# Optimization experiments

Measured on AMD Instinct MI355X. Metric: run time of the kernel, lower is better.

The kernel has to match this reference:

```python
import jax, jax.numpy as jnp
import numpy as np

N_NODES = 50000
N_EDGES = 800000
IN_DIM, HID_DIM, OUT_DIM = 512, 64, 40


def setup_inputs() -> dict:
    key = jax.random.key(0)
    k1, k2, k3, k4, k5 = jax.random.split(key, 5)
    x = jax.random.normal(k1, (N_NODES, IN_DIM), dtype=jnp.float32)
    src = jax.random.randint(k2, (N_EDGES,), 0, N_NODES, dtype=jnp.int64)
    dst = jax.random.randint(k3, (N_EDGES,), 0, N_NODES, dtype=jnp.int64)
    # Linear weights stored as [in, out] (equivalent to torch W.T), no bias.
    W1 = jax.random.normal(k4, (IN_DIM, HID_DIM), dtype=jnp.float32) * (1.0 / np.sqrt(IN_DIM))
    W2 = jax.random.normal(k5, (HID_DIM, OUT_DIM), dtype=jnp.float32) * (1.0 / np.sqrt(HID_DIM))
    return {"x": x, "src": src, "dst": dst, "W1": W1, "W2": W2}


def _gnn_layer(x, src, dst, W, n_nodes):
    # linear projection then sparse-adjacency aggregation:
    # out[i] = sum_{(j->i) in E} (x @ W)[j]
    h = x @ W                                   # [N, out_dim]
    return jax.ops.segment_sum(h[src], dst, num_segments=n_nodes)


def reference(x, src, dst, W1, W2):
    n = x.shape[0]
    h = _gnn_layer(x, src, dst, W1, n)          # [N, HID]
    h = jax.nn.relu(h)
    h = _gnn_layer(h, src, dst, W2, n)          # [N, OUT]
    return jax.nn.log_softmax(h, axis=1)
```

## Files before the change

kernel.cpp:

```cpp
#include <hip/hip_runtime.h>
#include <hip/hip_bf16.h>
#include <math.h>

constexpr int IN_DIM = 512;
constexpr int HID = 64;
constexpr int OUTD = 40;
constexpr int CAP = 64;

typedef __attribute__((ext_vector_type(8))) short bf16x8;
typedef __attribute__((ext_vector_type(4))) float floatx4;
typedef unsigned short ushort_t;

__device__ __forceinline__ unsigned short f2bf(float f) {
    unsigned u = __float_as_uint(f);
    u += 0x7fff + ((u >> 16) & 1);
    return (unsigned short)(u >> 16);
}

__device__ __forceinline__ unsigned pk2(float x, float y) {
    __hip_bfloat162 h = __float22bfloat162_rn(make_float2(x, y));
    return *reinterpret_cast<unsigned*>(&h);
}

#define GW4 asm volatile("s_waitcnt vmcnt(4)" ::: "memory")
#define GW0 asm volatile("s_waitcnt vmcnt(0)" ::: "memory")

__global__ __launch_bounds__(256) void w1t_fill_kernel(const float* __restrict__ W1,
                                                       const float* __restrict__ W2,
                                                       ushort_t* __restrict__ Wt,
                                                       ushort_t* __restrict__ W2tb,
                                                       const int* __restrict__ src,
                                                       const int* __restrict__ dst,
                                                       int* __restrict__ deg,
                                                       int* __restrict__ srcs, int E, int N) {
    int bid = blockIdx.x;
    if (bid < 128) {
        int tid = bid * 256 + threadIdx.x;
        int k = tid >> 6;
        int n = tid & 63;
        Wt[(size_t)((k >> 5) * 64 + n) * 32 + (k & 31)] = f2bf(W1[tid]);
    } else if (bid == 128) {
        for (int idx = threadIdx.x; idx < 3072; idx += 256) {
            int j = idx & 7;
            int l = (idx >> 3) & 63;
            int f = idx >> 9;
            int nt = f >> 1, ks = f & 1;
            int k = ks * 32 + (l >> 4) * 8 + j;
            int col = nt * 16 + (l & 15);
            float v = (col < OUTD) ? W2[k * OUTD + col] : 0.f;
            W2tb[idx] = f2bf(v);
        }
    } else {
        const int eb = bid - 129;
        const int part = eb & 7;
        const int slice = eb >> 3;
        const int PART = (N + 7) >> 3;
        const int lo = part * PART;
        const int hi = lo + PART;
        int e0 = (slice * 256 + (int)threadIdx.x) * 4;
        if (e0 + 3 < E) {
            int4 s4 = *(const int4*)&src[e0];
            int4 d4 = *(const int4*)&dst[e0];
            int p;
            if (d4.x >= lo && d4.x < hi) {
                p = atomicAdd(&deg[d4.x], 1); if (p < CAP) srcs[(d4.x << 6) + p] = s4.x;
            }
            if (d4.y >= lo && d4.y < hi) {
                p = atomicAdd(&deg[d4.y], 1); if (p < CAP) srcs[(d4.y << 6) + p] = s4.y;
            }
            if (d4.z >= lo && d4.z < hi) {
                p = atomicAdd(&deg[d4.z], 1); if (p < CAP) srcs[(d4.z << 6) + p] = s4.z;
            }
            if (d4.w >= lo && d4.w < hi) {
                p = atomicAdd(&deg[d4.w], 1); if (p < CAP) srcs[(d4.w << 6) + p] = s4.w;
            }
        } else {
            for (int i = 0; i < 4; ++i) {
                int e = e0 + i;
                if (e < E) {
                    int d = dst[e];
                    if (d >= lo && d < hi) {
                        int p = atomicAdd(&deg[d], 1);
                        if (p < CAP) srcs[(d << 6) + p] = src[e];
                    }
                }
            }
        }
    }
}

__global__ __launch_bounds__(128) void gemm1_kernel(const float* __restrict__ x,
                                                    const ushort_t* __restrict__ Wt,
                                                    ushort_t* __restrict__ h1b, int N) {
    __shared__ char lds[2 * 3 * 4096];
    const int lane = threadIdx.x & 63;
    const int wave = threadIdx.x >> 6;
    const int lm = lane & 15;
    const int quad = lane >> 4;

    const int row0 = (blockIdx.x * 2 + wave) * 16;
    char* wbase = lds + wave * 12288;
    char* b0 = wbase;
    char* b1 = wbase + 4096;
    char* b2 = wbase + 8192;

    const ushort_t* wB = Wt + lm * 32 + quad * 8;

    floatx4 acc0 = {0.f, 0.f, 0.f, 0.f};
    floatx4 acc1 = {0.f, 0.f, 0.f, 0.f};
    floatx4 acc2 = {0.f, 0.f, 0.f, 0.f};
    floatx4 acc3 = {0.f, 0.f, 0.f, 0.f};

    auto stage_chunk = [&](int c, char* buf) {
#pragma unroll
        for (int i = 0; i < 4; ++i) {
            int rr = i * 4 + (lane >> 4);
            int gr = row0 + rr;
            if (gr > N - 1) gr = N - 1;
            int g = (lane & 15) ^ (rr & 15);
            const float* gp = x + (size_t)gr * IN_DIM + c * 64 + g * 4;
            __builtin_amdgcn_global_load_lds((const void*)gp, (void*)(buf + i * 1024), 16, 0, 0);
        }
    };

    const int sz = (lm & 15) << 4;

    auto iter = [&](int c, const char* rbuf, char* sbuf, bool dostage, bool wait0) {
        if (wait0) { GW0; } else { GW4; }
        const ushort_t* wc0 = wB + (size_t)(c * 2) * 2048;
        const ushort_t* wc1 = wc0 + 2048;
        bf16x8 bA0 = *(const bf16x8*)(wc0);
        bf16x8 bA1 = *(const bf16x8*)(wc0 + 512);
        bf16x8 bA2 = *(const bf16x8*)(wc0 + 1024);
        bf16x8 bA3 = *(const bf16x8*)(wc0 + 1536);
        bf16x8 bB0 = *(const bf16x8*)(wc1);
        bf16x8 bB1 = *(const bf16x8*)(wc1 + 512);
        bf16x8 bB2 = *(const bf16x8*)(wc1 + 1024);
        bf16x8 bB3 = *(const bf16x8*)(wc1 + 1536);
        __builtin_amdgcn_sched_barrier(0);
        if (dostage) stage_chunk(c + 2, sbuf);
        __builtin_amdgcn_sched_barrier(0);
        const char* rp = rbuf + lm * 256;
        {
            float4 a0 = *(const float4*)(rp + (((quad * 2) << 4) ^ sz));
            float4 a1 = *(const float4*)(rp + (((quad * 2 + 1) << 4) ^ sz));
            union { bf16x8 v; unsigned u[4]; } af;
            af.u[0] = pk2(a0.x, a0.y);
            af.u[1] = pk2(a0.z, a0.w);
            af.u[2] = pk2(a1.x, a1.y);
            af.u[3] = pk2(a1.z, a1.w);
            acc0 = __builtin_amdgcn_mfma_f32_16x16x32_bf16(af.v, bA0, acc0, 0, 0, 0);
            acc1 = __builtin_amdgcn_mfma_f32_16x16x32_bf16(af.v, bA1, acc1, 0, 0, 0);
            acc2 = __builtin_amdgcn_mfma_f32_16x16x32_bf16(af.v, bA2, acc2, 0, 0, 0);
            acc3 = __builtin_amdgcn_mfma_f32_16x16x32_bf16(af.v, bA3, acc3, 0, 0, 0);
        }
        {
            float4 a0 = *(const float4*)(rp + (((8 + quad * 2) << 4) ^ sz));
            float4 a1 = *(const float4*)(rp + (((8 + quad * 2 + 1) << 4) ^ sz));
            union { bf16x8 v; unsigned u[4]; } af;
            af.u[0] = pk2(a0.x, a0.y);
            af.u[1] = pk2(a0.z, a0.w);
            af.u[2] = pk2(a1.x, a1.y);
            af.u[3] = pk2(a1.z, a1.w);
            acc0 = __builtin_amdgcn_mfma_f32_16x16x32_bf16(af.v, bB0, acc0, 0, 0, 0);
            acc1 = __builtin_amdgcn_mfma_f32_16x16x32_bf16(af.v, bB1, acc1, 0, 0, 0);
            acc2 = __builtin_amdgcn_mfma_f32_16x16x32_bf16(af.v, bB2, acc2, 0, 0, 0);
            acc3 = __builtin_amdgcn_mfma_f32_16x16x32_bf16(af.v, bB3, acc3, 0, 0, 0);
        }
    };

    stage_chunk(0, b0);
    stage_chunk(1, b1);

    iter(0, b0, b2, true, false);
    iter(1, b1, b0, true, false);
    iter(2, b2, b1, true, false);
    iter(3, b0, b2, true, false);
    iter(4, b1, b0, true, false);
    iter(5, b2, b1, true, false);
    iter(6, b0, b2, false, false);
    iter(7, b1, b2, false, true);

    const int rb = row0 + quad * 4;
#pragma unroll
    for (int reg = 0; reg < 4; ++reg) {
        int r = rb + reg;
        if (r < N) {
            ushort_t* hr = h1b + (size_t)r * HID + lm;
            hr[0]  = f2bf(acc0[reg]);
            hr[16] = f2bf(acc1[reg]);
            hr[32] = f2bf(acc2[reg]);
            hr[48] = f2bf(acc3[reg]);
        }
    }
}

template <int RELU>
__global__ __launch_bounds__(256) void agg_kernel(const ushort_t* __restrict__ hin,
                                                  const int* __restrict__ deg,
                                                  const int* __restrict__ srcs,
                                                  ushort_t* __restrict__ hout, int N) {
    int node = (blockIdx.x * 256 + threadIdx.x) >> 6;
    int lane = threadIdx.x & 63;
    if (node >= N) return;
    int dg = deg[node];
    if (dg > CAP) dg = CAP;
    int b = node << 6;
    int e = b + dg;
    const int half = lane >> 5;
    const int cp = lane & 31;
    float acc0 = 0.f, acc1 = 0.f;
    for (int j = b; j < e; j += 16) {
        int i0 = j + half * 8;
        int4 sa = *(const int4*)&srcs[i0];
        int4 sb = *(const int4*)&srcs[i0 + 4];
        int ss[8] = {sa.x, sa.y, sa.z, sa.w, sb.x, sb.y, sb.z, sb.w};
        unsigned u[8] = {0u, 0u, 0u, 0u, 0u, 0u, 0u, 0u};
#pragma unroll
        for (int t = 0; t < 8; ++t)
            if (i0 + t < e) u[t] = *(const unsigned*)&hin[(size_t)ss[t] * HID + cp * 2];
#pragma unroll
        for (int t = 0; t < 8; ++t) {
            acc0 += __uint_as_float(u[t] << 16);
            acc1 += __uint_as_float(u[t] & 0xffff0000u);
        }
    }
    acc0 += __shfl_xor(acc0, 32, 64);
    acc1 += __shfl_xor(acc1, 32, 64);
    if (half == 0) {
        float r0 = RELU ? fmaxf(acc0, 0.f) : acc0;
        float r1 = RELU ? fmaxf(acc1, 0.f) : acc1;
        *(unsigned*)&hout[(size_t)node * HID + cp * 2] = pk2(r0, r1);
    }
}

__global__ __launch_bounds__(256) void gemmlsm_kernel(const ushort_t* __restrict__ agg2b,
                                                      const ushort_t* __restrict__ W2tb,
                                                      float* __restrict__ out, int N) {
    const int lane = threadIdx.x & 63;
    const int wave = threadIdx.x >> 6;
    const int lm = lane & 15;
    const int quad = lane >> 4;
    const int row0 = (blockIdx.x * 4 + wave) * 16;

    int ar = row0 + lm;
    if (ar > N - 1) ar = N - 1;
    const ushort_t* ap = agg2b + (size_t)ar * HID + quad * 8;
    bf16x8 a0 = *(const bf16x8*)(ap);
    bf16x8 a1 = *(const bf16x8*)(ap + 32);

    const ushort_t* bp = W2tb + (size_t)lane * 8;
    bf16x8 b00 = *(const bf16x8*)(bp);
    bf16x8 b01 = *(const bf16x8*)(bp + 512);
    bf16x8 b10 = *(const bf16x8*)(bp + 1024);
    bf16x8 b11 = *(const bf16x8*)(bp + 1536);
    bf16x8 b20 = *(const bf16x8*)(bp + 2048);
    bf16x8 b21 = *(const bf16x8*)(bp + 2560);

    floatx4 c0 = {0.f, 0.f, 0.f, 0.f};
    floatx4 c1 = {0.f, 0.f, 0.f, 0.f};
    floatx4 c2 = {0.f, 0.f, 0.f, 0.f};
    c0 = __builtin_amdgcn_mfma_f32_16x16x32_bf16(a0, b00, c0, 0, 0, 0);
    c0 = __builtin_amdgcn_mfma_f32_16x16x32_bf16(a1, b01, c0, 0, 0, 0);
    c1 = __builtin_amdgcn_mfma_f32_16x16x32_bf16(a0, b10, c1, 0, 0, 0);
    c1 = __builtin_amdgcn_mfma_f32_16x16x32_bf16(a1, b11, c1, 0, 0, 0);
    c2 = __builtin_amdgcn_mfma_f32_16x16x32_bf16(a0, b20, c2, 0, 0, 0);
    c2 = __builtin_amdgcn_mfma_f32_16x16x32_bf16(a1, b21, c2, 0, 0, 0);

#pragma unroll
    for (int r = 0; r < 4; ++r) {
        float v0 = c0[r], v1 = c1[r], v2 = c2[r];
        float m = fmaxf(v0, v1);
        if (lm < 8) m = fmaxf(m, v2);
#pragma unroll
        for (int o = 8; o; o >>= 1) m = fmaxf(m, __shfl_xor(m, o, 64));
        float ex = expf(v0 - m) + expf(v1 - m) + ((lm < 8) ? expf(v2 - m) : 0.f);
#pragma unroll
        for (int o = 8; o; o >>= 1) ex += __shfl_xor(ex, o, 64);
        float ls = logf(ex);
        int row = row0 + quad * 4 + r;
        if (row < N) {
            float* orow = out + (size_t)row * OUTD;
            orow[lm] = v0 - m - ls;
            orow[16 + lm] = v1 - m - ls;
            if (lm < 8) orow[32 + lm] = v2 - m - ls;
        }
    }
}

extern "C" void kernel_launch(void* const* d_in, const int* in_sizes, int n_in,
                              void* d_out, int out_size, void* d_ws, size_t ws_size,
                              hipStream_t stream) {
    const float* x  = (const float*)d_in[0];
    const int*  src = (const int*)d_in[1];
    const int*  dst = (const int*)d_in[2];
    const float* W1 = (const float*)d_in[3];
    const float* W2 = (const float*)d_in[4];
    float* out = (float*)d_out;

    const int N = in_sizes[0] / IN_DIM;
    const int E = in_sizes[1];

    char* base = (char*)d_ws;
    ushort_t* Wt    = (ushort_t*)base;
    ushort_t* W2tb  = (ushort_t*)(base + 65536);
    ushort_t* h1b   = (ushort_t*)(base + 65536 + 8192);
    ushort_t* agg1b = h1b + (size_t)N * HID;
    ushort_t* agg2b = agg1b + (size_t)N * HID;
    int*   deg      = (int*)(agg2b + (size_t)N * HID);
    int*   srcs     = deg + N;

    hipMemsetAsync(deg, 0, (size_t)N * sizeof(int), stream);

    const int nSlices = (E + 1023) / 1024;
    const int edgeBlocks = nSlices * 8;
    w1t_fill_kernel<<<129 + edgeBlocks, 256, 0, stream>>>(W1, W2, Wt, W2tb, src, dst, deg,
                                                          srcs, E, N);

    gemm1_kernel<<<(N + 31) / 32, 128, 0, stream>>>(x, Wt, h1b, N);
    agg_kernel<1><<<(N * 64 + 255) / 256, 256, 0, stream>>>(h1b, deg, srcs, agg1b, N);
    agg_kernel<0><<<(N * 64 + 255) / 256, 256, 0, stream>>>(agg1b, deg, srcs, agg2b, N);
    gemmlsm_kernel<<<(N + 63) / 64, 256, 0, stream>>>(agg2b, W2tb, out, N);
}
```

Before: 271.1 us.

## Fuse edge bucketing into GEMM1 launch and replace memset with prep kernel

The memset of the degree array is replaced by a prep kernel that also converts the weights. Edge bucketing (atomic scatter into per-node source lists) now runs inside the GEMM1 launch, interleaved in groups of 72 blocks (8 GEMM, 64 fill), so the memory-bound scatter overlaps the GEMM. GEMM1 blocks grow to 4 waves (64 rows) with 48KB of LDS, which may reduce occupancy. The aim is to cut launch and serialization cost between the bucketing and GEMM phases.

```diff
diff --git a/kernel.cpp b/kernel.cpp
--- a/kernel.cpp
+++ b/kernel.cpp
@@ -25,14 +25,11 @@
 #define GW4 asm volatile("s_waitcnt vmcnt(4)" ::: "memory")
 #define GW0 asm volatile("s_waitcnt vmcnt(0)" ::: "memory")
 
-__global__ __launch_bounds__(256) void w1t_fill_kernel(const float* __restrict__ W1,
-                                                       const float* __restrict__ W2,
-                                                       ushort_t* __restrict__ Wt,
-                                                       ushort_t* __restrict__ W2tb,
-                                                       const int* __restrict__ src,
-                                                       const int* __restrict__ dst,
-                                                       int* __restrict__ deg,
-                                                       int* __restrict__ srcs, int E, int N) {
+__global__ __launch_bounds__(256) void prep_kernel(const float* __restrict__ W1,
+                                                   const float* __restrict__ W2,
+                                                   ushort_t* __restrict__ Wt,
+                                                   ushort_t* __restrict__ W2tb,
+                                                   int* __restrict__ deg, int N) {
     int bid = blockIdx.x;
     if (bid < 128) {
         int tid = bid * 256 + threadIdx.x;
@@ -51,9 +48,34 @@
             W2tb[idx] = f2bf(v);
         }
     } else {
-        const int eb = bid - 129;
-        const int part = eb & 7;
-        const int slice = eb >> 3;
+        int i = (bid - 129) * 1024 + (int)threadIdx.x * 4;
+        if (i + 3 < N) {
+            *(int4*)&deg[i] = make_int4(0, 0, 0, 0);
+        } else {
+            for (int t = 0; t < 4; ++t)
+                if (i + t < N) deg[i + t] = 0;
+        }
+    }
+}
+
+__global__ __launch_bounds__(256) void gemm1_fill_kernel(const float* __restrict__ x,
+                                                         const ushort_t* __restrict__ Wt,
+                                                         ushort_t* __restrict__ h1b,
+                                                         const int* __restrict__ src,
+                                                         const int* __restrict__ dst,
+                                                         int* __restrict__ deg,
+                                                         int* __restrict__ srcs,
+                                                         int E, int N, int nSlices) {
+    __shared__ char lds[4 * 3 * 4096];
+    const int bid = blockIdx.x;
+    const int grp = bid / 72;
+    const int rem = bid - grp * 72;
+
+    if (rem >= 8) {
+        const int fidx = grp * 64 + rem - 8;
+        if (fidx >= 8 * nSlices) return;
+        const int part = fidx & 7;
+        const int slice = fidx >> 3;
         const int PART = (N + 7) >> 3;
         const int lo = part * PART;
         const int hi = lo + PART;
@@ -86,19 +108,18 @@
                 }
             }
         }
-    }
-}
-
-__global__ __launch_bounds__(128) void gemm1_kernel(const float* __restrict__ x,
-                                                    const ushort_t* __restrict__ Wt,
-                                                    ushort_t* __restrict__ h1b, int N) {
-    __shared__ char lds[2 * 3 * 4096];
+        return;
+    }
+
+    const int gb = grp * 8 + rem;
+    if (gb * 64 >= N) return;
+
     const int lane = threadIdx.x & 63;
     const int wave = threadIdx.x >> 6;
     const int lm = lane & 15;
     const int quad = lane >> 4;
 
-    const int row0 = (blockIdx.x * 2 + wave) * 16;
+    const int row0 = gb * 64 + wave * 16;
     char* wbase = lds + wave * 12288;
     char* b0 = wbase;
     char* b1 = wbase + 4096;
@@ -310,14 +331,17 @@
     int*   deg      = (int*)(agg2b + (size_t)N * HID);
     int*   srcs     = deg + N;
 
-    hipMemsetAsync(deg, 0, (size_t)N * sizeof(int), stream);
+    const int degZeroBlocks = (N + 1023) / 1024;
+    prep_kernel<<<129 + degZeroBlocks, 256, 0, stream>>>(W1, W2, Wt, W2tb, deg, N);
 
     const int nSlices = (E + 1023) / 1024;
-    const int edgeBlocks = nSlices * 8;
-    w1t_fill_kernel<<<129 + edgeBlocks, 256, 0, stream>>>(W1, W2, Wt, W2tb, src, dst, deg,
-                                                          srcs, E, N);
-
-    gemm1_kernel<<<(N + 31) / 32, 128, 0, stream>>>(x, Wt, h1b, N);
+    const int nGemmB = (N + 63) / 64;
+    int nGroups = (nSlices * 8 + 63) / 64;
+    int g2 = (nGemmB + 7) / 8;
+    if (g2 > nGroups) nGroups = g2;
+    gemm1_fill_kernel<<<nGroups * 72, 256, 0, stream>>>(x, Wt, h1b, src, dst, deg, srcs,
+                                                        E, N, nSlices);
+
     agg_kernel<1><<<(N * 64 + 255) / 256, 256, 0, stream>>>(h1b, deg, srcs, agg1b, N);
     agg_kernel<0><<<(N * 64 + 255) / 256, 256, 0, stream>>>(agg1b, deg, srcs, agg2b, N);
     gemmlsm_kernel<<<(N + 63) / 64, 256, 0, stream>>>(agg2b, W2tb, out, N);
```

Result: faster. 259.1 us (-4.5%).
